# Kernel tuning notes

Hardware: AMD Instinct MI355X
Metric: run time of the kernel (lower is better)

The kernel has to match this reference:

```python
import jax, jax.numpy as jnp
import numpy as np

B, L, D, R = 8, 2048, 512, 512  # batch, seq, feature, n_rules


def setup_inputs() -> dict:
    key = jax.random.key(0)
    ks = jax.random.split(key, 6)
    query = jax.random.normal(ks[0], (B, L, D), dtype=jnp.float32)
    # to_q: Linear(D, D)
    Wq = jax.random.normal(ks[1], (D, D), dtype=jnp.float32) / np.sqrt(D)
    bq = jnp.zeros((D,), dtype=jnp.float32)
    # to_c: Linear(L, R)
    Wc = jax.random.normal(ks[2], (R, L), dtype=jnp.float32) / np.sqrt(L)
    bc = jnp.zeros((R,), dtype=jnp.float32)
    # fuzzy rule params, torch.rand init (uniform [0,1)); widths kept away from 0
    centers = jax.random.uniform(ks[3], (R, D), dtype=jnp.float32)
    widths = jax.random.uniform(ks[4], (R, D), dtype=jnp.float32, minval=0.1, maxval=1.0)
    return {"query": query, "Wq": Wq, "bq": bq, "Wc": Wc, "bc": bc,
            "centers": centers, "widths": widths}


def reference(query, Wq, bq, Wc, bc, centers, widths):
    # q = to_q(query)  (projection=True)
    q = query @ Wq.T + bq  # (B, L, D)
    # z[b,l,r] = -0.5 * mean_d (|q - c| / w)^2 ; abs is a no-op under the square,
    # so expand (q - c)^2 / w^2 into three GEMM-friendly terms (exact same math).
    inv_w2 = 1.0 / (widths * widths)                      # (R, D)
    qq = (q * q) @ inv_w2.T                               # (B, L, R)
    qc = q @ (centers * inv_w2).T                         # (B, L, R)
    cc = jnp.sum(centers * centers * inv_w2, axis=-1)     # (R,)
    z = -(0.5 / D) * (qq - 2.0 * qc + cc)                 # (B, L, R)
    Fss = jax.nn.softmax(z, axis=-1)                      # (B, L, R); dropout p=0
    # conq = to_c applied along the L axis of query, yielding (B, R, D)
    conq = jnp.einsum('bld,rl->brd', query, Wc) + bc[None, :, None]
    return Fss @ conq                                     # (B, L, D)
```

## Files before the change

### kernel.cpp

```cpp
#include <hip/hip_runtime.h>
#include <hip/hip_bf16.h>

constexpr int Bb = 8, Ls = 2048, Dd = 512, Rr = 512;
constexpr int M1 = Bb * Ls;

typedef _Float16 h8v __attribute__((ext_vector_type(8)));
typedef _Float16 h4v __attribute__((ext_vector_type(4)));
typedef float f4v __attribute__((ext_vector_type(4)));

__device__ __forceinline__ void async_copy16(const void* g, void* l) {
  __builtin_amdgcn_global_load_lds((const __attribute__((address_space(1))) unsigned int*)g,
                                   (__attribute__((address_space(3))) unsigned int*)l, 16, 0, 0);
}

__global__ __launch_bounds__(256) void prep_all(
    const float* __restrict__ q, _Float16* __restrict__ qs, _Float16* __restrict__ qt,
    const float* __restrict__ Wq, _Float16* __restrict__ wq,
    const float* __restrict__ Wc, _Float16* __restrict__ wc,
    const float* __restrict__ centers, const float* __restrict__ widths,
    _Float16* __restrict__ iwh, _Float16* __restrict__ c2h, float* __restrict__ cc,
    float* __restrict__ rowsum) {
  const int bid = blockIdx.x, tid = threadIdx.x;
  if (bid < 2048) {
    __shared__ float t[64][65];
    const int b = bid >> 8;
    const int l0 = ((bid >> 3) & 31) * 64;
    const int d0 = (bid & 7) * 64;
    const int r = tid >> 4, c4 = (tid & 15) * 4;
#pragma unroll
    for (int i = 0; i < 4; ++i) {
      const int l = r + i * 16;
      const float4 v = *(const float4*)&q[((long)b * Ls + l0 + l) * Dd + d0 + c4];
      t[l][c4] = v.x; t[l][c4 + 1] = v.y; t[l][c4 + 2] = v.z; t[l][c4 + 3] = v.w;
      h4v h = {(_Float16)v.x, (_Float16)v.y, (_Float16)v.z, (_Float16)v.w};
      *(h4v*)&qs[((long)b * Ls + l0 + l) * Dd + d0 + c4] = h;
    }
    __syncthreads();
#pragma unroll
    for (int i = 0; i < 4; ++i) {
      const int d = r + i * 16;
      h4v h = {(_Float16)t[c4][d], (_Float16)t[c4 + 1][d],
               (_Float16)t[c4 + 2][d], (_Float16)t[c4 + 3][d]};
      *(h4v*)&qt[((long)b * Dd + d0 + d) * Ls + l0 + c4] = h;
    }
  } else if (bid < 2304) {
    const int i = (bid - 2048) * 256 + tid;
    float4 v = *(const float4*)&Wq[(long)i * 4];
    h4v o = {(_Float16)v.x, (_Float16)v.y, (_Float16)v.z, (_Float16)v.w};
    *(h4v*)&wq[(long)i * 4] = o;
  } else if (bid < 3328) {
    const int i = (bid - 2304) * 256 + tid;
    float4 v = *(const float4*)&Wc[(long)i * 4];
    h4v o = {(_Float16)v.x, (_Float16)v.y, (_Float16)v.z, (_Float16)v.w};
    *(h4v*)&wc[(long)i * 4] = o;
  } else if (bid < 3456) {
    const int wave = tid >> 6, lane = tid & 63;
    const int r = (bid - 3328) * 4 + wave;
    float s = 0.f;
#pragma unroll
    for (int j = 0; j < 8; ++j) {
      const int d = j * 64 + lane;
      const float c = centers[(long)r * Dd + d];
      const float w = widths[(long)r * Dd + d];
      const float iw = 1.0f / (w * w);
      iwh[(long)r * Dd + d] = (_Float16)iw;
      c2h[(long)r * Dd + d] = (_Float16)(-2.0f * c * iw);
      s += c * c * iw;
    }
#pragma unroll
    for (int o = 32; o > 0; o >>= 1) s += __shfl_xor(s, o, 64);
    if (lane == 0) cc[r] = s;
  } else {
    const int i = (bid - 3456) * 256 + tid;
    ((float4*)rowsum)[i] = (float4){0.f, 0.f, 0.f, 0.f};
  }
}

template <int WM, int EPI>
__device__ __forceinline__ void gemm_body(
    const int lin, const int NX, const int NY, _Float16* __restrict__ smem,
    const _Float16* __restrict__ A, const _Float16* __restrict__ Bm,
    const float* __restrict__ bias, float* __restrict__ Cf, _Float16* __restrict__ Ch,
    const int Kext, const int ldA, const int ldB, const int ldC,
    const long sA, const long sB, const long sC) {
  constexpr int TM = WM * 32;
  _Float16* As = smem;
  _Float16* Bs = smem + TM * 64;

  const int xcd = lin & 7;
  const int wi = lin >> 3;
  const int x = wi % NX;
  const int yy = (wi / NX) * 8 + xcd;
  const int y = yy % NY;
  const int zz = yy / NY;
  const int n0 = x * 128;
  const int m0 = y * TM;
  const _Float16* Ab = A + (long)zz * sA;
  const _Float16* Bbp = Bm + (long)zz * sB;

  const int tid = threadIdx.x;
  const int wave = tid >> 6, lane = tid & 63;
  const int wm = wave >> 2, wn = wave & 3;
  const int quad = lane >> 4, tr = lane & 15;
  const int lrow = lane >> 2;
  const int lcol = (lane & 3) * 8;

  f4v acc[WM][2];
#pragma unroll
  for (int i = 0; i < WM; ++i)
#pragma unroll
    for (int j = 0; j < 2; ++j) acc[i][j] = (f4v){0.f, 0.f, 0.f, 0.f};

  for (int k0 = 0; k0 < Kext; k0 += 64) {
    __syncthreads();
#pragma unroll
    for (int c = wave; c < TM / 16; c += 8) {
      const long g = (long)(m0 + c * 16 + lrow) * ldA + k0 + lcol;
      async_copy16(Ab + g, &As[c * 512]);
      async_copy16(Ab + g + 32, &As[TM * 32 + c * 512]);
    }
#pragma unroll
    for (int c = wave; c < 8; c += 8) {
      const long g = (long)(n0 + c * 16 + lrow) * ldB + k0 + lcol;
      async_copy16(Bbp + g, &Bs[c * 512]);
      async_copy16(Bbp + g + 32, &Bs[4096 + c * 512]);
    }
    __syncthreads();

#pragma unroll
    for (int h = 0; h < 2; ++h) {
      h8v af[WM], bf[2];
#pragma unroll
      for (int i = 0; i < WM; ++i)
        af[i] = *(const h8v*)&As[h * (TM * 32) + (wm * (WM * 16) + i * 16 + tr) * 32 + quad * 8];
#pragma unroll
      for (int j = 0; j < 2; ++j)
        bf[j] = *(const h8v*)&Bs[h * 4096 + (wn * 32 + j * 16 + tr) * 32 + quad * 8];
#pragma unroll
      for (int i = 0; i < WM; ++i)
#pragma unroll
        for (int j = 0; j < 2; ++j)
          acc[i][j] = __builtin_amdgcn_mfma_f32_16x16x32_f16(af[i], bf[j], acc[i][j], 0, 0, 0);
    }
  }

  float* Cfb = Cf ? Cf + (long)zz * sC : nullptr;
  _Float16* Chb = Ch ? Ch + (long)zz * sC : nullptr;
#pragma unroll
  for (int i = 0; i < WM; ++i) {
    const int rbase = m0 + wm * (WM * 16) + i * 16 + quad * 4;
    float inv[4];
    if (EPI == 4) {
#pragma unroll
      for (int r = 0; r < 4; ++r) inv[r] = 1.0f / bias[(long)zz * Ls + rbase + r];
    }
#pragma unroll
    for (int j = 0; j < 2; ++j) {
      const int cg = n0 + wn * 32 + j * 16 + tr;
#pragma unroll
      for (int r = 0; r < 4; ++r) {
        const float v = acc[i][j][r];
        const long row = rbase + r;
        if (EPI == 2) {
          Chb[row * (long)ldC + cg] = (_Float16)(v + bias[cg]);
        } else if (EPI == 3) {
          Cfb[row * (long)ldC + cg] = v;
        } else if (EPI == 4) {
          Cfb[row * (long)ldC + cg] = v * inv[r];
        }
      }
    }
  }
}

template <int WM, int EPI>
__global__ __launch_bounds__(512, 4) void gemm_h(
    const _Float16* __restrict__ A, const _Float16* __restrict__ Bm,
    const float* __restrict__ bias, float* __restrict__ Cf,
    _Float16* __restrict__ Ch, int Kext, int ldA, int ldB, int ldC,
    long sA, long sB, long sC) {
  extern __shared__ _Float16 smem[];
  const int lin = ((int)blockIdx.z * (int)gridDim.y + (int)blockIdx.y) * (int)gridDim.x +
                  (int)blockIdx.x;
  gemm_body<WM, EPI>(lin, (int)gridDim.x, (int)gridDim.y, smem, A, Bm, bias, Cf, Ch,
                     Kext, ldA, ldB, ldC, sA, sB, sC);
}

__global__ __launch_bounds__(512, 4) void qgemm_conq(
    const _Float16* __restrict__ qs, const _Float16* __restrict__ wq,
    const float* __restrict__ bq, _Float16* __restrict__ q16,
    const _Float16* __restrict__ qt, const _Float16* __restrict__ wc,
    const float* __restrict__ bc, _Float16* __restrict__ cq) {
  extern __shared__ _Float16 smem[];
  const int bid = (int)blockIdx.x;
  if (bid < 256) {
    gemm_body<2, 2>(bid, 4, 64, smem, qt, wc, bc, nullptr, cq,
                    Ls, Ls, Ls, Rr, 0, 0, 0);
  } else {
    gemm_body<4, 2>(bid - 256, 4, 128, smem, qs, wq, bq, nullptr, q16,
                    Dd, Dd, Dd, Dd, 0, 0, 0);
  }
}

__global__ __launch_bounds__(512, 4) void zq_gemm(
    const _Float16* __restrict__ Q, const _Float16* __restrict__ Iw,
    const _Float16* __restrict__ C2, const float* __restrict__ cc,
    _Float16* __restrict__ Fh, float* __restrict__ rowsum) {
  __shared__ _Float16 As[2][128 * 32];
  __shared__ _Float16 B1[2][128 * 32];
  __shared__ _Float16 B2[2][128 * 32];
  __shared__ float rowpart[128][4];
  const int lin = (int)blockIdx.y * 4 + (int)blockIdx.x;
  const int xcd = lin & 7;
  const int wi = lin >> 3;
  const int x = wi % 4;
  const int yy = (wi / 4) * 8 + xcd;
  const int n0 = x * 128;
  const int m0 = yy * 128;

  const int tid = threadIdx.x;
  const int wave = tid >> 6, lane = tid & 63;
  const int wm = wave >> 2, wn = wave & 3;
  const int quad = lane >> 4, tr = lane & 15;
  const int lrow = lane >> 2;
  const int lcol = (lane & 3) * 8;

  f4v acc[4][2];
#pragma unroll
  for (int i = 0; i < 4; ++i)
#pragma unroll
    for (int j = 0; j < 2; ++j) acc[i][j] = (f4v){0.f, 0.f, 0.f, 0.f};

  for (int k0 = 0; k0 < 512; k0 += 64) {
    __syncthreads();
    {
      const long ga = (long)(m0 + wave * 16 + lrow) * 512 + k0 + lcol;
      async_copy16(Q + ga, &As[0][wave * 512]);
      async_copy16(Q + ga + 32, &As[1][wave * 512]);
      const long gb = (long)(n0 + wave * 16 + lrow) * 512 + k0 + lcol;
      async_copy16(Iw + gb, &B1[0][wave * 512]);
      async_copy16(Iw + gb + 32, &B1[1][wave * 512]);
      async_copy16(C2 + gb, &B2[0][wave * 512]);
      async_copy16(C2 + gb + 32, &B2[1][wave * 512]);
    }
    __syncthreads();

#pragma unroll
    for (int h = 0; h < 2; ++h) {
      h8v af[4], af2[4], b1[2], b2[2];
#pragma unroll
      for (int i = 0; i < 4; ++i) {
        af[i] = *(const h8v*)&As[h][(wm * 64 + i * 16 + tr) * 32 + quad * 8];
        af2[i] = af[i] * af[i];
      }
#pragma unroll
      for (int j = 0; j < 2; ++j) {
        b1[j] = *(const h8v*)&B1[h][(wn * 32 + j * 16 + tr) * 32 + quad * 8];
        b2[j] = *(const h8v*)&B2[h][(wn * 32 + j * 16 + tr) * 32 + quad * 8];
      }
#pragma unroll
      for (int i = 0; i < 4; ++i)
#pragma unroll
        for (int j = 0; j < 2; ++j) {
          acc[i][j] = __builtin_amdgcn_mfma_f32_16x16x32_f16(af2[i], b1[j], acc[i][j], 0, 0, 0);
          acc[i][j] = __builtin_amdgcn_mfma_f32_16x16x32_f16(af[i], b2[j], acc[i][j], 0, 0, 0);
        }
    }
  }

  constexpr float zs = -0.0009765625f;
#pragma unroll
  for (int i = 0; i < 4; ++i) {
    float ps[2][4];
#pragma unroll
    for (int j = 0; j < 2; ++j) {
      const int cg = n0 + wn * 32 + j * 16 + tr;
      const float ccv = cc[cg];
#pragma unroll
      for (int r = 0; r < 4; ++r) ps[j][r] = __expf((acc[i][j][r] + ccv) * zs);
    }
    const int rbase = m0 + wm * 64 + i * 16 + quad * 4;
#pragma unroll
    for (int j = 0; j < 2; ++j) {
      const int cg = n0 + wn * 32 + j * 16 + tr;
#pragma unroll
      for (int r = 0; r < 4; ++r)
        Fh[(long)(rbase + r) * 512 + cg] = (_Float16)ps[j][r];
    }
#pragma unroll
    for (int r = 0; r < 4; ++r) {
      float s = ps[0][r] + ps[1][r];
#pragma unroll
      for (int o = 8; o > 0; o >>= 1) s += __shfl_xor(s, o, 64);
      if (tr == 0) rowpart[wm * 64 + i * 16 + quad * 4 + r][wn] = s;
    }
  }
  __syncthreads();
  if (tid < 128) {
    const float s = rowpart[tid][0] + rowpart[tid][1] + rowpart[tid][2] + rowpart[tid][3];
    atomicAdd(&rowsum[m0 + tid], s);
  }
}

extern "C" void kernel_launch(void* const* d_in, const int* in_sizes, int n_in,
                              void* d_out, int out_size, void* d_ws, size_t ws_size,
                              hipStream_t stream) {
  const float* query   = (const float*)d_in[0];
  const float* Wq      = (const float*)d_in[1];
  const float* bq      = (const float*)d_in[2];
  const float* Wc      = (const float*)d_in[3];
  const float* bc      = (const float*)d_in[4];
  const float* centers = (const float*)d_in[5];
  const float* widths  = (const float*)d_in[6];
  float* out = (float*)d_out;

  char* base = (char*)d_ws;
  auto alloc = [&](size_t bytes) {
    char* p = base;
    base += (bytes + 255) & ~(size_t)255;
    return p;
  };
  _Float16* qs  = (_Float16*)alloc((size_t)M1 * Dd * 2);
  _Float16* qt  = (_Float16*)alloc((size_t)M1 * Dd * 2);
  _Float16* q16 = (_Float16*)alloc((size_t)M1 * Dd * 2);
  _Float16* fs  = (_Float16*)alloc((size_t)M1 * Rr * 2);
  _Float16* wq  = (_Float16*)alloc((size_t)Dd * Dd * 2);
  _Float16* wc  = (_Float16*)alloc((size_t)Rr * Ls * 2);
  _Float16* iwh = (_Float16*)alloc((size_t)Rr * Dd * 2);
  _Float16* c2h = (_Float16*)alloc((size_t)Rr * Dd * 2);
  float*    cc  = (float*)alloc((size_t)Rr * 4);
  float*    rowsum = (float*)alloc((size_t)M1 * 4);
  _Float16* cq  = (_Float16*)alloc((size_t)Bb * Dd * Rr * 2);

  prep_all<<<3472, 256, 0, stream>>>(query, qs, qt, Wq, wq, Wc, wc,
                                     centers, widths, iwh, c2h, cc, rowsum);

  qgemm_conq<<<768, 512, 32768, stream>>>(qs, wq, bq, q16, qt, wc, bc, cq);

  zq_gemm<<<dim3(Rr / 128, M1 / 128, 1), 512, 0, stream>>>(q16, iwh, c2h, cc, fs, rowsum);

  gemm_h<4, 4><<<dim3(Dd / 128, Ls / 128, Bb), 512, 32768, stream>>>(
      fs, cq, rowsum, out, nullptr, Rr, Rr, Rr, Dd,
      (long)Ls * Rr, (long)Dd * Rr, (long)Ls * Dd);
}
```

Baseline: 168.2 us.

## Co-schedule conq GEMM with the fuzzy-rule GEMM instead of the q projection

The conq GEMM (Wc applied along L) now runs in the same launch as the z/softmax-numerator GEMM. Before, it shared a launch with the q projection, and the q projection now gets its own gemm_h launch. The zq body is refactored into a device function that uses dynamic shared memory, so both block types can share one kernel. The aim is to balance per-launch work, since the zq GEMM depends on q16 but not on conq. The kernel now requests 51200 bytes of dynamic shared memory, up from 32768, which may lower occupancy for the conq blocks.

Result: slower. 172.0 us (+2.3%).

```diff
diff --git a/kernel.cpp b/kernel.cpp
--- a/kernel.cpp
+++ b/kernel.cpp
@@ -186,9 +186,112 @@
                      Kext, ldA, ldB, ldC, sA, sB, sC);
 }
 
-__global__ __launch_bounds__(512, 4) void qgemm_conq(
-    const _Float16* __restrict__ qs, const _Float16* __restrict__ wq,
-    const float* __restrict__ bq, _Float16* __restrict__ q16,
+__device__ __forceinline__ void zq_body(
+    const int lin, _Float16* __restrict__ smem,
+    const _Float16* __restrict__ Q, const _Float16* __restrict__ Iw,
+    const _Float16* __restrict__ C2, const float* __restrict__ cc,
+    _Float16* __restrict__ Fh, float* __restrict__ rowsum) {
+  _Float16* As = smem;
+  _Float16* B1 = smem + 8192;
+  _Float16* B2 = smem + 16384;
+  float* rowpart = (float*)(smem + 24576);
+
+  const int xcd = lin & 7;
+  const int wi = lin >> 3;
+  const int x = wi % 4;
+  const int yy = (wi / 4) * 8 + xcd;
+  const int n0 = x * 128;
+  const int m0 = yy * 128;
+
+  const int tid = threadIdx.x;
+  const int wave = tid >> 6, lane = tid & 63;
+  const int wm = wave >> 2, wn = wave & 3;
+  const int quad = lane >> 4, tr = lane & 15;
+  const int lrow = lane >> 2;
+  const int lcol = (lane & 3) * 8;
+
+  f4v acc[4][2];
+#pragma unroll
+  for (int i = 0; i < 4; ++i)
+#pragma unroll
+    for (int j = 0; j < 2; ++j) acc[i][j] = (f4v){0.f, 0.f, 0.f, 0.f};
+
+  for (int k0 = 0; k0 < 512; k0 += 64) {
+    __syncthreads();
+    {
+      const long ga = (long)(m0 + wave * 16 + lrow) * 512 + k0 + lcol;
+      async_copy16(Q + ga, &As[wave * 512]);
+      async_copy16(Q + ga + 32, &As[4096 + wave * 512]);
+      const long gb = (long)(n0 + wave * 16 + lrow) * 512 + k0 + lcol;
+      async_copy16(Iw + gb, &B1[wave * 512]);
+      async_copy16(Iw + gb + 32, &B1[4096 + wave * 512]);
+      async_copy16(C2 + gb, &B2[wave * 512]);
+      async_copy16(C2 + gb + 32, &B2[4096 + wave * 512]);
+    }
+    __syncthreads();
+
+#pragma unroll
+    for (int h = 0; h < 2; ++h) {
+      h8v af[4], af2[4], b1[2], b2[2];
+#pragma unroll
+      for (int i = 0; i < 4; ++i) {
+        af[i] = *(const h8v*)&As[h * 4096 + (wm * 64 + i * 16 + tr) * 32 + quad * 8];
+        af2[i] = af[i] * af[i];
+      }
+#pragma unroll
+      for (int j = 0; j < 2; ++j) {
+        b1[j] = *(const h8v*)&B1[h * 4096 + (wn * 32 + j * 16 + tr) * 32 + quad * 8];
+        b2[j] = *(const h8v*)&B2[h * 4096 + (wn * 32 + j * 16 + tr) * 32 + quad * 8];
+      }
+#pragma unroll
+      for (int i = 0; i < 4; ++i)
+#pragma unroll
+        for (int j = 0; j < 2; ++j) {
+          acc[i][j] = __builtin_amdgcn_mfma_f32_16x16x32_f16(af2[i], b1[j], acc[i][j], 0, 0, 0);
+          acc[i][j] = __builtin_amdgcn_mfma_f32_16x16x32_f16(af[i], b2[j], acc[i][j], 0, 0, 0);
+        }
+    }
+  }
+
+  constexpr float zs = -0.0009765625f;
+#pragma unroll
+  for (int i = 0; i < 4; ++i) {
+    float ps[2][4];
+#pragma unroll
+    for (int j = 0; j < 2; ++j) {
+      const int cg = n0 + wn * 32 + j * 16 + tr;
+      const float ccv = cc[cg];
+#pragma unroll
+      for (int r = 0; r < 4; ++r) ps[j][r] = __expf((acc[i][j][r] + ccv) * zs);
+    }
+    const int rbase = m0 + wm * 64 + i * 16 + quad * 4;
+#pragma unroll
+    for (int j = 0; j < 2; ++j) {
+      const int cg = n0 + wn * 32 + j * 16 + tr;
+#pragma unroll
+      for (int r = 0; r < 4; ++r)
+        Fh[(long)(rbase + r) * 512 + cg] = (_Float16)ps[j][r];
+    }
+#pragma unroll
+    for (int r = 0; r < 4; ++r) {
+      float s = ps[0][r] + ps[1][r];
+#pragma unroll
+      for (int o = 8; o > 0; o >>= 1) s += __shfl_xor(s, o, 64);
+      if (tr == 0) rowpart[(wm * 64 + i * 16 + quad * 4 + r) * 4 + wn] = s;
+    }
+  }
+  __syncthreads();
+  if (tid < 128) {
+    const float s = rowpart[tid * 4] + rowpart[tid * 4 + 1] +
+                    rowpart[tid * 4 + 2] + rowpart[tid * 4 + 3];
+    atomicAdd(&rowsum[m0 + tid], s);
+  }
+}
+
+__global__ __launch_bounds__(512, 4) void zq_conq(
+    const _Float16* __restrict__ q16, const _Float16* __restrict__ iwh,
+    const _Float16* __restrict__ c2h, const float* __restrict__ cc,
+    _Float16* __restrict__ fs, float* __restrict__ rowsum,
     const _Float16* __restrict__ qt, const _Float16* __restrict__ wc,
     const float* __restrict__ bc, _Float16* __restrict__ cq) {
   extern __shared__ _Float16 smem[];
@@ -197,108 +300,7 @@
     gemm_body<2, 2>(bid, 4, 64, smem, qt, wc, bc, nullptr, cq,
                     Ls, Ls, Ls, Rr, 0, 0, 0);
   } else {
-    gemm_body<4, 2>(bid - 256, 4, 128, smem, qs, wq, bq, nullptr, q16,
-                    Dd, Dd, Dd, Dd, 0, 0, 0);
-  }
-}
-
-__global__ __launch_bounds__(512, 4) void zq_gemm(
-    const _Float16* __restrict__ Q, const _Float16* __restrict__ Iw,
-    const _Float16* __restrict__ C2, const float* __restrict__ cc,
-    _Float16* __restrict__ Fh, float* __restrict__ rowsum) {
-  __shared__ _Float16 As[2][128 * 32];
-  __shared__ _Float16 B1[2][128 * 32];
-  __shared__ _Float16 B2[2][128 * 32];
-  __shared__ float rowpart[128][4];
-  const int lin = (int)blockIdx.y * 4 + (int)blockIdx.x;
-  const int xcd = lin & 7;
-  const int wi = lin >> 3;
-  const int x = wi % 4;
-  const int yy = (wi / 4) * 8 + xcd;
-  const int n0 = x * 128;
-  const int m0 = yy * 128;
-
-  const int tid = threadIdx.x;
-  const int wave = tid >> 6, lane = tid & 63;
-  const int wm = wave >> 2, wn = wave & 3;
-  const int quad = lane >> 4, tr = lane & 15;
-  const int lrow = lane >> 2;
-  const int lcol = (lane & 3) * 8;
-
-  f4v acc[4][2];
-#pragma unroll
-  for (int i = 0; i < 4; ++i)
-#pragma unroll
-    for (int j = 0; j < 2; ++j) acc[i][j] = (f4v){0.f, 0.f, 0.f, 0.f};
-
-  for (int k0 = 0; k0 < 512; k0 += 64) {
-    __syncthreads();
-    {
-      const long ga = (long)(m0 + wave * 16 + lrow) * 512 + k0 + lcol;
-      async_copy16(Q + ga, &As[0][wave * 512]);
-      async_copy16(Q + ga + 32, &As[1][wave * 512]);
-      const long gb = (long)(n0 + wave * 16 + lrow) * 512 + k0 + lcol;
-      async_copy16(Iw + gb, &B1[0][wave * 512]);
-      async_copy16(Iw + gb + 32, &B1[1][wave * 512]);
-      async_copy16(C2 + gb, &B2[0][wave * 512]);
-      async_copy16(C2 + gb + 32, &B2[1][wave * 512]);
-    }
-    __syncthreads();
-
-#pragma unroll
-    for (int h = 0; h < 2; ++h) {
-      h8v af[4], af2[4], b1[2], b2[2];
-#pragma unroll
-      for (int i = 0; i < 4; ++i) {
-        af[i] = *(const h8v*)&As[h][(wm * 64 + i * 16 + tr) * 32 + quad * 8];
-        af2[i] = af[i] * af[i];
-      }
-#pragma unroll
-      for (int j = 0; j < 2; ++j) {
-        b1[j] = *(const h8v*)&B1[h][(wn * 32 + j * 16 + tr) * 32 + quad * 8];
-        b2[j] = *(const h8v*)&B2[h][(wn * 32 + j * 16 + tr) * 32 + quad * 8];
-      }
-#pragma unroll
-      for (int i = 0; i < 4; ++i)
-#pragma unroll
-        for (int j = 0; j < 2; ++j) {
-          acc[i][j] = __builtin_amdgcn_mfma_f32_16x16x32_f16(af2[i], b1[j], acc[i][j], 0, 0, 0);
-          acc[i][j] = __builtin_amdgcn_mfma_f32_16x16x32_f16(af[i], b2[j], acc[i][j], 0, 0, 0);
-        }
-    }
-  }
-
-  constexpr float zs = -0.0009765625f;
-#pragma unroll
-  for (int i = 0; i < 4; ++i) {
-    float ps[2][4];
-#pragma unroll
-    for (int j = 0; j < 2; ++j) {
-      const int cg = n0 + wn * 32 + j * 16 + tr;
-      const float ccv = cc[cg];
-#pragma unroll
-      for (int r = 0; r < 4; ++r) ps[j][r] = __expf((acc[i][j][r] + ccv) * zs);
-    }
-    const int rbase = m0 + wm * 64 + i * 16 + quad * 4;
-#pragma unroll
-    for (int j = 0; j < 2; ++j) {
-      const int cg = n0 + wn * 32 + j * 16 + tr;
-#pragma unroll
-      for (int r = 0; r < 4; ++r)
-        Fh[(long)(rbase + r) * 512 + cg] = (_Float16)ps[j][r];
-    }
-#pragma unroll
-    for (int r = 0; r < 4; ++r) {
-      float s = ps[0][r] + ps[1][r];
-#pragma unroll
-      for (int o = 8; o > 0; o >>= 1) s += __shfl_xor(s, o, 64);
-      if (tr == 0) rowpart[wm * 64 + i * 16 + quad * 4 + r][wn] = s;
-    }
-  }
-  __syncthreads();
-  if (tid < 128) {
-    const float s = rowpart[tid][0] + rowpart[tid][1] + rowpart[tid][2] + rowpart[tid][3];
-    atomicAdd(&rowsum[m0 + tid], s);
+    zq_body(bid - 256, smem, q16, iwh, c2h, cc, fs, rowsum);
   }
 }
 
@@ -335,9 +337,11 @@
   prep_all<<<3472, 256, 0, stream>>>(query, qs, qt, Wq, wq, Wc, wc,
                                      centers, widths, iwh, c2h, cc, rowsum);
 
-  qgemm_conq<<<768, 512, 32768, stream>>>(qs, wq, bq, q16, qt, wc, bc, cq);
-
-  zq_gemm<<<dim3(Rr / 128, M1 / 128, 1), 512, 0, stream>>>(q16, iwh, c2h, cc, fs, rowsum);
+  gemm_h<4, 2><<<dim3(Dd / 128, M1 / 128, 1), 512, 32768, stream>>>(
+      qs, wq, bq, nullptr, q16, Dd, Dd, Dd, Dd, 0, 0, 0);
+
+  zq_conq<<<768, 512, 51200, stream>>>(q16, iwh, c2h, cc, fs, rowsum,
+                                       qt, wc, bc, cq);
 
   gemm_h<4, 4><<<dim3(Dd / 128, Ls / 128, Bb), 512, 32768, stream>>>(
       fs, cq, rowsum, out, nullptr, Rr, Rr, Rr, Dd,
```
